# Performance work log

Hardware: AMD Instinct MI355X
Metric: run time of the kernel (lower is better)

## Reference

```python
import jax, jax.numpy as jnp
import numpy as np

EPS = 1e-6
B, K, D = 512, 1024, 256  # batch, out_features, in_features


def setup_inputs() -> dict:
    key = jax.random.key(0)
    kx, kp, ka = jax.random.split(key, 3)
    x = jax.random.normal(kx, (B, D), dtype=jnp.float32)
    # project inputs inside the Poincare ball (norm < 1)
    x = 0.7 * x / (1.0 + jnp.linalg.norm(x, axis=-1, keepdims=True))
    # module inits p, a ~ U(-0.001, 0.001); tiny norms are already inside the ball
    p = jax.random.uniform(kp, (K, D), minval=-0.001, maxval=0.001, dtype=jnp.float32)
    a = jax.random.uniform(ka, (K, D), minval=-0.001, maxval=0.001, dtype=jnp.float32)
    return {"x": x, "p": p, "a": a}


def _mobius_add(u, v):
    # Mobius addition on the Poincare ball (c=1), broadcasting over leading dims
    u2 = jnp.sum(u * u, axis=-1, keepdims=True)
    v2 = jnp.sum(v * v, axis=-1, keepdims=True)
    uv = jnp.sum(u * v, axis=-1, keepdims=True)
    num = (1.0 + 2.0 * uv + v2) * u + (1.0 - u2) * v
    den = 1.0 + 2.0 * uv + u2 * v2
    return num / (den + EPS)


def reference(x, p, a):
    # x: [B, D]; p, a: [K, D]
    p2 = jnp.sum(p * p, axis=-1, keepdims=True)           # [K, 1]
    # parallel transport of a from origin to p: PT_{0->p}(a) = (1 - ||p||^2) a
    a_pt = (1.0 - p2) * a                                  # [K, D]
    lam_p = 2.0 / (1.0 - p2 + EPS)                         # [K, 1] conformal factor at p
    # broadcast hyperplane math instead of materializing .repeat() copies
    z = _mobius_add(-p[None, :, :], x[:, None, :])         # [B, K, D] = (-p) (+) x
    z2 = jnp.sum(z * z, axis=-1)                           # [B, K]
    za = jnp.einsum('bkd,kd->bk', z, a_pt)                 # [B, K]
    na = jnp.linalg.norm(a_pt, axis=-1)                    # [K]
    # Ganea hyperbolic MLR logit: lam_p * ||a|| * asinh(2<z,a> / ((1-||z||^2)||a||))
    logits = lam_p[:, 0][None, :] * na[None, :] * jnp.arcsinh(
        2.0 * za / ((1.0 - z2) * na[None, :] + EPS)
    )
    return logits  # [B, K]
```

## Files before the change

### kernel.cpp

```cpp
#include <hip/hip_runtime.h>
#include <math.h>

#define B_ 512
#define K_ 1024
#define D_ 256
#define EPS_ 1e-6f

#define BM 64
#define BN 32
#define BK 32
#define NG 4
#define JG (BK / NG)
#define XLD (BM + 4)
#define PLD (BN + 4)

__global__ __launch_bounds__(1024) void hyp_mlr_kernel(
    const float* __restrict__ x,
    const float* __restrict__ p,
    const float* __restrict__ a,
    float* __restrict__ out)
{
    __shared__ __align__(16) float Xs[2][BK][XLD];
    __shared__ __align__(16) float Ps[2][BK][PLD];
    __shared__ __align__(16) float As[2][BK][PLD];
    __shared__ float Red[256][27];

    const int t  = threadIdx.x;
    const int u  = t & 255;
    const int g  = t >> 8;
    const int tx = u & 15;
    const int ty = u >> 4;
    const int k0 = blockIdx.x * BN;
    const int b0 = blockIdx.y * BM;

    int lrow, lcol;
    const float* gsrc;
    if (t < 512)      { lrow = t >> 3;          lcol = (t & 7) * 4; gsrc = &x[(b0 + lrow) * D_ + lcol]; }
    else if (t < 768) { const int q = t - 512;  lrow = q >> 3; lcol = (q & 7) * 4; gsrc = &p[(k0 + lrow) * D_ + lcol]; }
    else              { const int q = t - 768;  lrow = q >> 3; lcol = (q & 7) * 4; gsrc = &a[(k0 + lrow) * D_ + lcol]; }

    auto stage = [&](int buf, float4 v) {
        if (t < 512) {
            Xs[buf][lcol+0][lrow] = v.x; Xs[buf][lcol+1][lrow] = v.y;
            Xs[buf][lcol+2][lrow] = v.z; Xs[buf][lcol+3][lrow] = v.w;
        } else if (t < 768) {
            Ps[buf][lcol+0][lrow] = v.x; Ps[buf][lcol+1][lrow] = v.y;
            Ps[buf][lcol+2][lrow] = v.z; Ps[buf][lcol+3][lrow] = v.w;
        } else {
            As[buf][lcol+0][lrow] = v.x; As[buf][lcol+1][lrow] = v.y;
            As[buf][lcol+2][lrow] = v.z; As[buf][lcol+3][lrow] = v.w;
        }
    };

    float dotp[4][2] = {{0.f,0.f},{0.f,0.f},{0.f,0.f},{0.f,0.f}};
    float dota[4][2] = {{0.f,0.f},{0.f,0.f},{0.f,0.f},{0.f,0.f}};
    float x2a[4] = {0.f,0.f,0.f,0.f};
    float p2a[2] = {0.f,0.f};
    float a2a[2] = {0.f,0.f};
    float paa[2] = {0.f,0.f};

    stage(0, *(const float4*)gsrc);
    __syncthreads();

    int cur = 0;
    for (int kk = 0; kk < D_; kk += BK) {
        float4 nv;
        const bool hn = (kk + BK) < D_;
        if (hn) nv = *(const float4*)(gsrc + kk + BK);

#pragma unroll
        for (int j = 0; j < JG; ++j) {
            const int d = g * JG + j;
            float4 xv = *(const float4*)&Xs[cur][d][ty * 4];
            float2 pv = *(const float2*)&Ps[cur][d][tx * 2];
            float2 av = *(const float2*)&As[cur][d][tx * 2];
            float xr[4] = {xv.x, xv.y, xv.z, xv.w};
            float pr[2] = {pv.x, pv.y};
            float ar[2] = {av.x, av.y};
#pragma unroll
            for (int i = 0; i < 4; ++i) {
                x2a[i] = fmaf(xr[i], xr[i], x2a[i]);
#pragma unroll
                for (int c = 0; c < 2; ++c) {
                    dotp[i][c] = fmaf(xr[i], pr[c], dotp[i][c]);
                    dota[i][c] = fmaf(xr[i], ar[c], dota[i][c]);
                }
            }
#pragma unroll
            for (int c = 0; c < 2; ++c) {
                p2a[c] = fmaf(pr[c], pr[c], p2a[c]);
                a2a[c] = fmaf(ar[c], ar[c], a2a[c]);
                paa[c] = fmaf(pr[c], ar[c], paa[c]);
            }
        }

        if (hn) {
            stage(cur ^ 1, nv);
            __syncthreads();
            cur ^= 1;
        }
    }

    float pay[26];
#pragma unroll
    for (int i = 0; i < 4; ++i) {
        pay[i * 2 + 0] = dotp[i][0]; pay[i * 2 + 1] = dotp[i][1];
        pay[8 + i * 2 + 0] = dota[i][0]; pay[8 + i * 2 + 1] = dota[i][1];
        pay[16 + i] = x2a[i];
    }
    pay[20] = p2a[0]; pay[21] = p2a[1];
    pay[22] = a2a[0]; pay[23] = a2a[1];
    pay[24] = paa[0]; pay[25] = paa[1];

    __syncthreads();
    if (g == 1) {
#pragma unroll
        for (int j = 0; j < 26; ++j) Red[u][j] = pay[j];
    }
    __syncthreads();
    if (g == 2) {
#pragma unroll
        for (int j = 0; j < 26; ++j) Red[u][j] += pay[j];
    }
    __syncthreads();
    if (g == 3) {
#pragma unroll
        for (int j = 0; j < 26; ++j) Red[u][j] += pay[j];
    }
    __syncthreads();

    if (g == 0) {
#pragma unroll
        for (int j = 0; j < 26; ++j) pay[j] += Red[u][j];

#pragma unroll
        for (int i = 0; i < 4; ++i) {
            const int b = b0 + ty * 4 + i;
            const float x2 = pay[16 + i];
            float res[2];
#pragma unroll
            for (int c = 0; c < 2; ++c) {
                const float p2 = pay[20 + c];
                const float a2 = pay[22 + c];
                const float pa = pay[24 + c];
                const float dt = pay[i * 2 + c];
                const float xa = pay[8 + i * 2 + c];

                const float beta  = 1.0f - p2;
                const float alpha = 1.0f + x2 - 2.0f * dt;
                const float den   = 1.0f - 2.0f * dt + p2 * x2;
                const float rg    = 1.0f / (den + EPS_);
                const float z2    = (alpha * alpha * p2 - 2.0f * alpha * beta * dt
                                     + beta * beta * x2) * rg * rg;
                const float za    = beta * (beta * xa - alpha * pa) * rg;
                const float na    = beta * sqrtf(a2);
                const float lam   = 2.0f / (beta + EPS_);
                const float arg   = 2.0f * za / ((1.0f - z2) * na + EPS_);
                res[c] = lam * na * asinhf(arg);
            }
            *(float2*)&out[b * K_ + k0 + tx * 2] = make_float2(res[0], res[1]);
        }
    }
}

extern "C" void kernel_launch(void* const* d_in, const int* in_sizes, int n_in,
                              void* d_out, int out_size, void* d_ws, size_t ws_size,
                              hipStream_t stream) {
    const float* x = (const float*)d_in[0];
    const float* p = (const float*)d_in[1];
    const float* a = (const float*)d_in[2];
    float* out = (float*)d_out;

    dim3 grid(K_ / BN, B_ / BM);
    dim3 block(1024);
    hyp_mlr_kernel<<<grid, block, 0, stream>>>(x, p, a, out);
}
```

Baseline: 71.31 us.

## Replace FP32 FMA dot products with split-bf16 MFMA matrix cores

```diff
diff --git a/kernel.cpp b/kernel.cpp
--- a/kernel.cpp
+++ b/kernel.cpp
@@ -9,157 +9,166 @@
 #define BM 64
 #define BN 32
 #define BK 32
-#define NG 4
-#define JG (BK / NG)
-#define XLD (BM + 4)
-#define PLD (BN + 4)
+#define STR 40
 
-__global__ __launch_bounds__(1024) void hyp_mlr_kernel(
+using short8  = __attribute__((ext_vector_type(8))) short;
+using floatx4 = __attribute__((ext_vector_type(4))) float;
+
+__device__ __forceinline__ unsigned short f2bf(float f) {
+    unsigned int u = __float_as_uint(f);
+    u += 0x7FFFu + ((u >> 16) & 1u);
+    return (unsigned short)(u >> 16);
+}
+__device__ __forceinline__ float bf2f(unsigned short h) {
+    return __uint_as_float((unsigned int)h << 16);
+}
+
+__global__ __launch_bounds__(512) void hyp_mlr_mfma(
     const float* __restrict__ x,
     const float* __restrict__ p,
     const float* __restrict__ a,
     float* __restrict__ out)
 {
-    __shared__ __align__(16) float Xs[2][BK][XLD];
-    __shared__ __align__(16) float Ps[2][BK][PLD];
-    __shared__ __align__(16) float As[2][BK][PLD];
-    __shared__ float Red[256][27];
+    __shared__ __align__(16) unsigned short Xh[2][BM][STR];
+    __shared__ __align__(16) unsigned short Xl[2][BM][STR];
+    __shared__ __align__(16) unsigned short Ph[2][BN][STR];
+    __shared__ __align__(16) unsigned short Pl[2][BN][STR];
+    __shared__ __align__(16) unsigned short Ah[2][BN][STR];
+    __shared__ __align__(16) unsigned short Al[2][BN][STR];
+    __shared__ float  x2s[BM];
+    __shared__ float4 scal[BN];
 
-    const int t  = threadIdx.x;
-    const int u  = t & 255;
-    const int g  = t >> 8;
-    const int tx = u & 15;
-    const int ty = u >> 4;
-    const int k0 = blockIdx.x * BN;
-    const int b0 = blockIdx.y * BM;
+    const int t    = threadIdx.x;
+    const int lane = t & 63;
+    const int wave = t >> 6;
+    const int k0   = blockIdx.x * BN;
+    const int b0   = blockIdx.y * BM;
 
-    int lrow, lcol;
-    const float* gsrc;
-    if (t < 512)      { lrow = t >> 3;          lcol = (t & 7) * 4; gsrc = &x[(b0 + lrow) * D_ + lcol]; }
-    else if (t < 768) { const int q = t - 512;  lrow = q >> 3; lcol = (q & 7) * 4; gsrc = &p[(k0 + lrow) * D_ + lcol]; }
-    else              { const int q = t - 768;  lrow = q >> 3; lcol = (q & 7) * 4; gsrc = &a[(k0 + lrow) * D_ + lcol]; }
+    const bool isx = (t < 256);
+    int srow, scol;
+    const float *gp0, *gp1;
+    if (isx) {
+        srow = t >> 2; scol = (t & 3) * 8;
+        gp0 = x + (b0 + srow) * D_ + scol;
+        gp1 = gp0 + 4;
+    } else {
+        const int q = t - 256;
+        srow = q >> 3; scol = (q & 7) * 4;
+        gp0 = p + (k0 + srow) * D_ + scol;
+        gp1 = a + (k0 + srow) * D_ + scol;
+    }
 
-    auto stage = [&](int buf, float4 v) {
-        if (t < 512) {
-            Xs[buf][lcol+0][lrow] = v.x; Xs[buf][lcol+1][lrow] = v.y;
-            Xs[buf][lcol+2][lrow] = v.z; Xs[buf][lcol+3][lrow] = v.w;
-        } else if (t < 768) {
-            Ps[buf][lcol+0][lrow] = v.x; Ps[buf][lcol+1][lrow] = v.y;
-            Ps[buf][lcol+2][lrow] = v.z; Ps[buf][lcol+3][lrow] = v.w;
+    float s0 = 0.f, s1 = 0.f, s2 = 0.f;
+
+    auto cvt_store = [&](int buf, float4 v0, float4 v1) {
+        if (isx) {
+            float e[8] = {v0.x, v0.y, v0.z, v0.w, v1.x, v1.y, v1.z, v1.w};
+            unsigned int hp[4], lp[4];
+#pragma unroll
+            for (int j = 0; j < 4; ++j) {
+                const float e0 = e[2 * j], e1 = e[2 * j + 1];
+                const unsigned short h0 = f2bf(e0), h1 = f2bf(e1);
+                hp[j] = (unsigned int)h0 | ((unsigned int)h1 << 16);
+                lp[j] = (unsigned int)f2bf(e0 - bf2f(h0))
+                      | ((unsigned int)f2bf(e1 - bf2f(h1)) << 16);
+                s0 = fmaf(e0, e0, fmaf(e1, e1, s0));
+            }
+            *(uint4*)&Xh[buf][srow][scol] = make_uint4(hp[0], hp[1], hp[2], hp[3]);
+            *(uint4*)&Xl[buf][srow][scol] = make_uint4(lp[0], lp[1], lp[2], lp[3]);
         } else {
-            As[buf][lcol+0][lrow] = v.x; As[buf][lcol+1][lrow] = v.y;
-            As[buf][lcol+2][lrow] = v.z; As[buf][lcol+3][lrow] = v.w;
+            float ep[4] = {v0.x, v0.y, v0.z, v0.w};
+            float ea[4] = {v1.x, v1.y, v1.z, v1.w};
+            unsigned int hp[2], lp[2], ha[2], la[2];
+#pragma unroll
+            for (int j = 0; j < 2; ++j) {
+                const float pe0 = ep[2 * j], pe1 = ep[2 * j + 1];
+                const float ae0 = ea[2 * j], ae1 = ea[2 * j + 1];
+                const unsigned short hp0 = f2bf(pe0), hp1 = f2bf(pe1);
+                const unsigned short ha0 = f2bf(ae0), ha1 = f2bf(ae1);
+                hp[j] = (unsigned int)hp0 | ((unsigned int)hp1 << 16);
+                lp[j] = (unsigned int)f2bf(pe0 - bf2f(hp0))
+                      | ((unsigned int)f2bf(pe1 - bf2f(hp1)) << 16);
+                ha[j] = (unsigned int)ha0 | ((unsigned int)ha1 << 16);
+                la[j] = (unsigned int)f2bf(ae0 - bf2f(ha0))
+                      | ((unsigned int)f2bf(ae1 - bf2f(ha1)) << 16);
+                s0 = fmaf(pe0, pe0, fmaf(pe1, pe1, s0));
+                s1 = fmaf(ae0, ae0, fmaf(ae1, ae1, s1));
+                s2 = fmaf(pe0, ae0, fmaf(pe1, ae1, s2));
+            }
+            *(uint2*)&Ph[buf][srow][scol] = make_uint2(hp[0], hp[1]);
+            *(uint2*)&Pl[buf][srow][scol] = make_uint2(lp[0], lp[1]);
+            *(uint2*)&Ah[buf][srow][scol] = make_uint2(ha[0], ha[1]);
+            *(uint2*)&Al[buf][srow][scol] = make_uint2(la[0], la[1]);
         }
     };
 
-    float dotp[4][2] = {{0.f,0.f},{0.f,0.f},{0.f,0.f},{0.f,0.f}};
-    float dota[4][2] = {{0.f,0.f},{0.f,0.f},{0.f,0.f},{0.f,0.f}};
-    float x2a[4] = {0.f,0.f,0.f,0.f};
-    float p2a[2] = {0.f,0.f};
-    float a2a[2] = {0.f,0.f};
-    float paa[2] = {0.f,0.f};
+    const int wm = wave & 3, wn = wave >> 2;
+    const int m0 = wm * 16, n0 = wn * 16;
+    const int lr = lane & 15, lg = lane >> 4;
 
-    stage(0, *(const float4*)gsrc);
+    floatx4 accD = {0.f, 0.f, 0.f, 0.f};
+    floatx4 accA = {0.f, 0.f, 0.f, 0.f};
+
+    cvt_store(0, *(const float4*)gp0, *(const float4*)gp1);
     __syncthreads();
 
-    int cur = 0;
-    for (int kk = 0; kk < D_; kk += BK) {
-        float4 nv;
-        const bool hn = (kk + BK) < D_;
-        if (hn) nv = *(const float4*)(gsrc + kk + BK);
-
+    int buf = 0;
 #pragma unroll
-        for (int j = 0; j < JG; ++j) {
-            const int d = g * JG + j;
-            float4 xv = *(const float4*)&Xs[cur][d][ty * 4];
-            float2 pv = *(const float2*)&Ps[cur][d][tx * 2];
-            float2 av = *(const float2*)&As[cur][d][tx * 2];
-            float xr[4] = {xv.x, xv.y, xv.z, xv.w};
-            float pr[2] = {pv.x, pv.y};
-            float ar[2] = {av.x, av.y};
-#pragma unroll
-            for (int i = 0; i < 4; ++i) {
-                x2a[i] = fmaf(xr[i], xr[i], x2a[i]);
-#pragma unroll
-                for (int c = 0; c < 2; ++c) {
-                    dotp[i][c] = fmaf(xr[i], pr[c], dotp[i][c]);
-                    dota[i][c] = fmaf(xr[i], ar[c], dota[i][c]);
-                }
-            }
-#pragma unroll
-            for (int c = 0; c < 2; ++c) {
-                p2a[c] = fmaf(pr[c], pr[c], p2a[c]);
-                a2a[c] = fmaf(ar[c], ar[c], a2a[c]);
-                paa[c] = fmaf(pr[c], ar[c], paa[c]);
-            }
+    for (int s = 0; s < D_ / BK; ++s) {
+        float4 nv0, nv1;
+        if (s < D_ / BK - 1) {
+            nv0 = *(const float4*)(gp0 + (s + 1) * BK);
+            nv1 = *(const float4*)(gp1 + (s + 1) * BK);
         }
 
-        if (hn) {
-            stage(cur ^ 1, nv);
-            __syncthreads();
-            cur ^= 1;
-        }
+        const short8 xh = *(const short8*)&Xh[buf][m0 + lr][lg * 8];
+        const short8 xl = *(const short8*)&Xl[buf][m0 + lr][lg * 8];
+        const short8 ph = *(const short8*)&Ph[buf][n0 + lr][lg * 8];
+        const short8 pl = *(const short8*)&Pl[buf][n0 + lr][lg * 8];
+        const short8 ah = *(const short8*)&Ah[buf][n0 + lr][lg * 8];
+        const short8 al = *(const short8*)&Al[buf][n0 + lr][lg * 8];
+        accD = __builtin_amdgcn_mfma_f32_16x16x32_bf16(xh, ph, accD, 0, 0, 0);
+        accA = __builtin_amdgcn_mfma_f32_16x16x32_bf16(xh, ah, accA, 0, 0, 0);
+        accD = __builtin_amdgcn_mfma_f32_16x16x32_bf16(xh, pl, accD, 0, 0, 0);
+        accA = __builtin_amdgcn_mfma_f32_16x16x32_bf16(xh, al, accA, 0, 0, 0);
+        accD = __builtin_amdgcn_mfma_f32_16x16x32_bf16(xl, ph, accD, 0, 0, 0);
+        accA = __builtin_amdgcn_mfma_f32_16x16x32_bf16(xl, ah, accA, 0, 0, 0);
+
+        if (s < D_ / BK - 1) cvt_store(buf ^ 1, nv0, nv1);
+        __syncthreads();
+        buf ^= 1;
     }
 
-    float pay[26];
-#pragma unroll
-    for (int i = 0; i < 4; ++i) {
-        pay[i * 2 + 0] = dotp[i][0]; pay[i * 2 + 1] = dotp[i][1];
-        pay[8 + i * 2 + 0] = dota[i][0]; pay[8 + i * 2 + 1] = dota[i][1];
-        pay[16 + i] = x2a[i];
-    }
-    pay[20] = p2a[0]; pay[21] = p2a[1];
-    pay[22] = a2a[0]; pay[23] = a2a[1];
-    pay[24] = paa[0]; pay[25] = paa[1];
-
-    __syncthreads();
-    if (g == 1) {
-#pragma unroll
-        for (int j = 0; j < 26; ++j) Red[u][j] = pay[j];
-    }
-    __syncthreads();
-    if (g == 2) {
-#pragma unroll
-        for (int j = 0; j < 26; ++j) Red[u][j] += pay[j];
-    }
-    __syncthreads();
-    if (g == 3) {
-#pragma unroll
-        for (int j = 0; j < 26; ++j) Red[u][j] += pay[j];
+    if (isx) {
+        s0 += __shfl_xor(s0, 1);
+        s0 += __shfl_xor(s0, 2);
+        if ((t & 3) == 0) x2s[srow] = s0;
+    } else {
+        s0 += __shfl_xor(s0, 1); s0 += __shfl_xor(s0, 2); s0 += __shfl_xor(s0, 4);
+        s1 += __shfl_xor(s1, 1); s1 += __shfl_xor(s1, 2); s1 += __shfl_xor(s1, 4);
+        s2 += __shfl_xor(s2, 1); s2 += __shfl_xor(s2, 2); s2 += __shfl_xor(s2, 4);
+        if (((t - 256) & 7) == 0) {
+            const float beta = 1.f - s0;
+            scal[srow] = make_float4(s0, s2, beta * sqrtf(s1), beta);
+        }
     }
     __syncthreads();
 
-    if (g == 0) {
+    const float4 sc  = scal[n0 + lr];
+    const float  lam = 2.f / (sc.w + EPS_);
 #pragma unroll
-        for (int j = 0; j < 26; ++j) pay[j] += Red[u][j];
-
-#pragma unroll
-        for (int i = 0; i < 4; ++i) {
-            const int b = b0 + ty * 4 + i;
-            const float x2 = pay[16 + i];
-            float res[2];
-#pragma unroll
-            for (int c = 0; c < 2; ++c) {
-                const float p2 = pay[20 + c];
-                const float a2 = pay[22 + c];
-                const float pa = pay[24 + c];
-                const float dt = pay[i * 2 + c];
-                const float xa = pay[8 + i * 2 + c];
-
-                const float beta  = 1.0f - p2;
-                const float alpha = 1.0f + x2 - 2.0f * dt;
-                const float den   = 1.0f - 2.0f * dt + p2 * x2;
-                const float rg    = 1.0f / (den + EPS_);
-                const float z2    = (alpha * alpha * p2 - 2.0f * alpha * beta * dt
-                                     + beta * beta * x2) * rg * rg;
-                const float za    = beta * (beta * xa - alpha * pa) * rg;
-                const float na    = beta * sqrtf(a2);
-                const float lam   = 2.0f / (beta + EPS_);
-                const float arg   = 2.0f * za / ((1.0f - z2) * na + EPS_);
-                res[c] = lam * na * asinhf(arg);
-            }
-            *(float2*)&out[b * K_ + k0 + tx * 2] = make_float2(res[0], res[1]);
-        }
+    for (int i = 0; i < 4; ++i) {
+        const int   r    = m0 + lg * 4 + i;
+        const float x2v  = x2s[r];
+        const float dt   = accD[i];
+        const float xa   = accA[i];
+        const float alpha = 1.f + x2v - 2.f * dt;
+        const float rg    = 1.f / (1.f - 2.f * dt + sc.x * x2v + EPS_);
+        const float z2    = (alpha * alpha * sc.x - 2.f * alpha * sc.w * dt
+                             + sc.w * sc.w * x2v) * rg * rg;
+        const float za    = sc.w * (sc.w * xa - alpha * sc.y) * rg;
+        const float arg   = 2.f * za / ((1.f - z2) * sc.z + EPS_);
+        out[(b0 + r) * K_ + k0 + n0 + lr] = lam * sc.z * asinhf(arg);
     }
 }
 
@@ -172,6 +181,6 @@
     float* out = (float*)d_out;
 
     dim3 grid(K_ / BN, B_ / BM);
-    dim3 block(1024);
-    hyp_mlr_kernel<<<grid, block, 0, stream>>>(x, p, a, out);
+    dim3 block(512);
+    hyp_mlr_mfma<<<grid, block, 0, stream>>>(x, p, a, out);
 }
```

After: 68.11 us. -4.5%, faster.
